# Kernel tuning notes

Hardware: AMD Instinct MI355X
Metric: run time of the kernel (lower is better)

The kernel has to match this reference:

```python
import jax, jax.numpy as jnp
import numpy as np

B, S, HID = 4, 4096, 2048
H = 16            # num_attention_heads
P = 256           # page_size
D = HID // H      # head_dim = 128
N = S // P        # num pages = 16
SCALE = D ** -0.5


def setup_inputs() -> dict:
    key = jax.random.key(0)
    ks = jax.random.split(key, 9)
    w = lambda k: (jax.random.normal(k, (HID, HID), jnp.float32) * 0.02)
    return {
        "hidden_states": jax.random.normal(ks[0], (B, S, HID), jnp.float32),
        "Wq": w(ks[1]), "bq": jnp.zeros((HID,), jnp.float32),
        "Wk": w(ks[2]), "bk": jnp.zeros((HID,), jnp.float32),
        "Wv": w(ks[3]), "bv": jnp.zeros((HID,), jnp.float32),
        "Wo": w(ks[4]), "bo": jnp.zeros((HID,), jnp.float32),
    }


def _heads(y):
    # (B,S,HID) -> (B,H,S,D)  [mirrors _reshape]
    return jnp.transpose(y.reshape(B, S, H, D), (0, 2, 1, 3))


def _paged(x):
    # torch: x.unfold(2, P, P) -> (B,H,N,D,P); then .reshape(-1,H,P,D)
    # reinterprets the row-major flat buffer. Reproduce exactly.
    u = jnp.swapaxes(x.reshape(B, H, N, P, D), -1, -2)  # (B,H,N,D,P)
    return u.reshape(B * N, H, P, D)


def reference(hidden_states, Wq, bq, Wk, bk, Wv, bv, Wo, bo):
    q = _heads(hidden_states @ Wq.T + bq)
    k = _heads(hidden_states @ Wk.T + bk)
    v = _heads(hidden_states @ Wv.T + bv)
    q, k, v = _paged(q), _paged(k), _paged(v)  # (B*N, H, P, D) each

    scores = jnp.einsum("xhqd,xhkd->xhqk", q, k) * SCALE  # (B*N,H,P,P)
    probs = jax.nn.softmax(scores, axis=-1)
    ctx = jnp.einsum("xhqk,xhkd->xhqd", probs, v)         # (B*N,H,P,D)

    # ctx.transpose(1,2).view(b, -1, hidden)
    ctx = jnp.transpose(ctx, (0, 2, 1, 3)).reshape(B, N * P, HID)
    return ctx @ Wo.T + bo
```

## Files before the change

### kernel.cpp

```cpp
#include <hip/hip_runtime.h>


typedef unsigned short u16;
typedef unsigned int u32;
typedef __attribute__((ext_vector_type(8))) __bf16 bf16x8;
typedef __attribute__((ext_vector_type(4))) float f32x4;
typedef __attribute__((ext_vector_type(8))) u16 u16x8;

struct alignas(8) U4 { u16 x, y, z, w; };

#define SCALE_ 0.08838834764831845f

__device__ __forceinline__ u16 f2bf(float f) {
  union { float f; u32 u; } v; v.f = f;
  u32 r = v.u + 0x7fffu + ((v.u >> 16) & 1u);
  return (u16)(r >> 16);
}

__device__ __forceinline__ void glds16(const void* g, void* l) {
  __builtin_amdgcn_global_load_lds(
      (const __attribute__((address_space(1))) u32*)g,
      (__attribute__((address_space(3))) u32*)l, 16, 0, 0);
}

__global__ void cvt_kernel(const float* __restrict__ src, u16* __restrict__ dst, int n4) {
  int i = blockIdx.x * 256 + threadIdx.x;
  if (i >= n4) return;
  float4 f = ((const float4*)src)[i];
  U4 o = { f2bf(f.x), f2bf(f.y), f2bf(f.z), f2bf(f.w) };
  ((U4*)dst)[i] = o;
}

__global__ void cvtw_kernel(const float* __restrict__ s0, const float* __restrict__ s1,
                            const float* __restrict__ s2, const float* __restrict__ s3,
                            u16* __restrict__ d0, int n4) {
  const int w = blockIdx.y;
  const float* src = (w == 0) ? s0 : (w == 1) ? s1 : (w == 2) ? s2 : s3;
  u16* dst = d0 + (size_t)w * 4194304;
  int i = blockIdx.x * 256 + threadIdx.x;
  if (i >= n4) return;
  float4 f = ((const float4*)src)[i];
  U4 o = { f2bf(f.x), f2bf(f.y), f2bf(f.z), f2bf(f.w) };
  ((U4*)dst)[i] = o;
}


#define MFMA_Q(AF, BF, MB, NB) do { \
  _Pragma("unroll") for (int mt_ = 0; mt_ < 4; ++mt_) \
  _Pragma("unroll") for (int nt_ = 0; nt_ < 2; ++nt_) \
  _Pragma("unroll") for (int kh_ = 0; kh_ < 2; ++kh_) \
    acc[(MB)+mt_][(NB)+nt_] = __builtin_amdgcn_mfma_f32_16x16x32_bf16( \
      AF[mt_][kh_], BF[nt_][kh_], acc[(MB)+mt_][(NB)+nt_], 0, 0, 0); \
} while (0)

#define LDA(F, MTB, BUF) do { \
  _Pragma("unroll") for (int mt_ = 0; mt_ < 4; ++mt_) { \
    F[mt_][0] = *(const bf16x8*)(aRd0 + (BUF)*65536 + ((MTB)+mt_)*2048); \
    F[mt_][1] = *(const bf16x8*)(aRd1 + (BUF)*65536 + ((MTB)+mt_)*2048); \
  } } while (0)

#define LDB(F, NTB, BUF) do { \
  _Pragma("unroll") for (int nt_ = 0; nt_ < 2; ++nt_) { \
    F[nt_][0] = *(const bf16x8*)(bRd0 + (BUF)*65536 + ((NTB)+nt_)*2048); \
    F[nt_][1] = *(const bf16x8*)(bRd1 + (BUF)*65536 + ((NTB)+nt_)*2048); \
  } } while (0)

#define STAGE_A(BUF, H, KK) do { \
  glds16(Asrc + (size_t)((H)*128) * 2048 + (KK), dstA + (BUF)*65536 + (H)*16384); \
  glds16(Asrc + (size_t)((H)*128 + 64) * 2048 + (KK), dstA + (BUF)*65536 + (H)*16384 + 8192); \
} while (0)

#define STAGE_B(BUF, H, KK) do { \
  glds16(Bsrc + (size_t)((H)*128) * 2048 + (KK), dstB + (BUF)*65536 + (H)*16384); \
  glds16(Bsrc + (size_t)((H)*128 + 64) * 2048 + (KK), dstB + (BUF)*65536 + (H)*16384 + 8192); \
} while (0)

#define PH_ENTER() do { \
  __builtin_amdgcn_s_barrier(); \
  asm volatile("s_waitcnt lgkmcnt(0)" ::: "memory"); \
  __builtin_amdgcn_sched_barrier(0); \
  __builtin_amdgcn_s_setprio(1); \
} while (0)

#define PH_EXIT() do { \
  __builtin_amdgcn_s_setprio(0); \
  __builtin_amdgcn_sched_barrier(0); \
  __builtin_amdgcn_s_barrier(); \
} while (0)

#define PH_EXIT_VM(N) do { \
  __builtin_amdgcn_s_setprio(0); \
  __builtin_amdgcn_sched_barrier(0); \
  asm volatile("s_waitcnt vmcnt(" #N ")" ::: "memory"); \
  __builtin_amdgcn_s_barrier(); \
} while (0)

#define LGKM_HINT() asm volatile("s_waitcnt lgkmcnt(8)" ::: "memory")

__global__ __launch_bounds__(512, 2) void gemm_kernel(
    const u16* __restrict__ A,
    const u16* __restrict__ W0, const u16* __restrict__ W1, const u16* __restrict__ W2,
    const float* __restrict__ b0, const float* __restrict__ b1, const float* __restrict__ b2,
    void* __restrict__ o0, void* __restrict__ o1, void* __restrict__ o2,
    int md0, int md1, int md2)
{
  extern __shared__ char Sm[];
  const int g = blockIdx.y;
  const u16* Bw     = (g == 0) ? W0 : (g == 1) ? W1 : W2;
  const float* bias = (g == 0) ? b0 : (g == 1) ? b1 : b2;
  void* outp        = (g == 0) ? o0 : (g == 1) ? o1 : o2;
  const int mode    = (g == 0) ? md0 : (g == 1) ? md1 : md2;

  const int tid  = threadIdx.x;
  const int lane = tid & 63;
  const int wid  = tid >> 6;
  const int L    = lane & 15;
  const int quad = lane >> 4;
  const int wm   = wid >> 2;
  const int wn   = wid & 3;
  const int bid = blockIdx.x;
  const int xcd = bid & 7;
  const int idx = bid >> 3;
  const int m0 = (xcd * 8 + (idx & 7)) << 8;
  const int n0 = (idx >> 3) << 8;

  const int srow = tid >> 3;
  const int scs  = (tid & 7) ^ (srow & 7);
  const u16* Asrc = A  + (size_t)(m0 + srow) * 2048 + scs * 8;
  const u16* Bsrc = Bw + (size_t)(n0 + srow) * 2048 + scs * 8;
  char* dstA = Sm + tid * 16;
  char* dstB = Sm + 32768 + tid * 16;

  const int xA = ((quad ^ (L & 7)) << 4);
  const char* aRd0 = Sm + (wm * 128 + L) * 128 + xA;
  const char* aRd1 = Sm + (wm * 128 + L) * 128 + (xA ^ 64);
  const char* bRd0 = Sm + 32768 + (wn * 64 + L) * 128 + xA;
  const char* bRd1 = Sm + 32768 + (wn * 64 + L) * 128 + (xA ^ 64);

  f32x4 acc[8][4];
#pragma unroll
  for (int i = 0; i < 8; ++i)
#pragma unroll
    for (int j = 0; j < 4; ++j)
      acc[i][j] = f32x4{0.f, 0.f, 0.f, 0.f};

  bf16x8 aLo[4][2], aHi[4][2], bLo[2][2], bHi[2][2];

  STAGE_A(0, 0, 0);
  STAGE_A(0, 1, 0);
  STAGE_B(0, 0, 0);
  STAGE_B(0, 1, 0);
  STAGE_A(1, 0, 64);
  STAGE_A(1, 1, 64);
  STAGE_B(1, 0, 64);
  STAGE_B(1, 1, 64);
  asm volatile("s_waitcnt vmcnt(8)" ::: "memory");
  __builtin_amdgcn_s_barrier();

#pragma unroll 1
  for (int it = 0; it < 16; ++it) {
    const int kb = it * 128;
    LDA(aLo, 0, 0); LDB(bLo, 0, 0);
    LGKM_HINT();
    PH_ENTER();
    MFMA_Q(aLo, bLo, 0, 0);
    PH_EXIT();
    LDA(aHi, 4, 0); LDB(bHi, 2, 0);
    LGKM_HINT();
    PH_ENTER();
    MFMA_Q(aLo, bHi, 0, 2);
    PH_EXIT();
    if (it < 15) { STAGE_A(0, 0, kb + 128); STAGE_A(0, 1, kb + 128); }
    PH_ENTER();
    MFMA_Q(aHi, bLo, 4, 0);
    PH_EXIT();
    if (it < 15) { STAGE_B(0, 0, kb + 128); STAGE_B(0, 1, kb + 128); }
    PH_ENTER();
    MFMA_Q(aHi, bHi, 4, 2);
    if (it < 15) { PH_EXIT_VM(8); } else { PH_EXIT_VM(0); }
    LDA(aLo, 0, 1); LDB(bLo, 0, 1);
    LGKM_HINT();
    PH_ENTER();
    MFMA_Q(aLo, bLo, 0, 0);
    PH_EXIT();
    LDA(aHi, 4, 1); LDB(bHi, 2, 1);
    LGKM_HINT();
    PH_ENTER();
    MFMA_Q(aLo, bHi, 0, 2);
    PH_EXIT();
    if (it < 15) { STAGE_A(1, 0, kb + 192); STAGE_A(1, 1, kb + 192); }
    PH_ENTER();
    MFMA_Q(aHi, bLo, 4, 0);
    PH_EXIT();
    if (it < 15) { STAGE_B(1, 0, kb + 192); STAGE_B(1, 1, kb + 192); }
    PH_ENTER();
    MFMA_Q(aHi, bHi, 4, 2);
    if (it < 15) { PH_EXIT_VM(8); } else { PH_EXIT(); }
  }

#pragma unroll
  for (int nt = 0; nt < 4; ++nt) {
    const int c = n0 + wn * 64 + nt * 16 + L;
    const float bv = bias[c];
    const int h = c >> 7, d = c & 127;
#pragma unroll
    for (int mt = 0; mt < 8; ++mt) {
      const int sg = m0 + wm * 128 + mt * 16 + (quad << 2);
      const int b   = sg >> 12;
      const int s   = sg & 4095;
      const int npg = (s >> 8) & 15;
      const int half = (s >> 7) & 1;
      const int plo  = s & 127;
      const f32x4 v = acc[mt][nt];
      const size_t bb = ((size_t)((b * 16 + h) * 16 + npg)) << 15;
      if (mode == 0) {
        U4 o = { f2bf(v[0] + bv), f2bf(v[1] + bv), f2bf(v[2] + bv), f2bf(v[3] + bv) };
        *(U4*)((u16*)outp + bb + (size_t)(2 * d + half) * 128 + plo) = o;
      } else if (mode == 1) {
        u16* o16 = (u16*)outp + bb + 2 * d + half;
        o16[(size_t)(plo + 0) * 256] = f2bf(v[0] + bv);
        o16[(size_t)(plo + 1) * 256] = f2bf(v[1] + bv);
        o16[(size_t)(plo + 2) * 256] = f2bf(v[2] + bv);
        o16[(size_t)(plo + 3) * 256] = f2bf(v[3] + bv);
      } else {
        float* of = (float*)outp + (size_t)sg * 2048 + c;
        of[0]    = v[0] + bv;
        of[2048] = v[1] + bv;
        of[4096] = v[2] + bv;
        of[6144] = v[3] + bv;
      }
    }
  }
}

__global__ __launch_bounds__(1024, 4) void attn_kernel(
    const u16* __restrict__ Qp, const u16* __restrict__ Kp,
    const u16* __restrict__ Vt, u16* __restrict__ ctx)
{
  __shared__ u16 Sm[32768];
  const int tid  = threadIdx.x;
  const int wid  = tid >> 6;
  const int lane = tid & 63;
  const int L    = lane & 15;
  const int quad = lane >> 4;
  const int pg   = blockIdx.x;
  const int x2 = pg >> 4, h2 = pg & 15;
  const int q0 = wid * 16;

  const char* Qb = (const char*)(Qp + (size_t)pg * 32768);
  const char* Kb = (const char*)(Kp + (size_t)pg * 32768);
  const char* Vb = (const char*)(Vt + (size_t)pg * 32768);

#pragma unroll
  for (int r = 0; r < 4; ++r) {
    const int u = tid + (r << 10);
    const int row = u >> 4, cc = u & 15;
    glds16(Kb + (size_t)(row * 16 + (cc ^ (row & 15))) * 16, (char*)Sm + u * 16);
  }

  bf16x8 qf[4];
#pragma unroll
  for (int kt = 0; kt < 4; ++kt)
    qf[kt] = *(const bf16x8*)(Qb + (q0 + L) * 256 + kt * 64 + quad * 16);

  __syncthreads();

  f32x4 st[16];
#pragma unroll
  for (int mt = 0; mt < 16; ++mt) st[mt] = f32x4{0.f, 0.f, 0.f, 0.f};
#pragma unroll
  for (int kt = 0; kt < 4; ++kt) {
    const int c = kt * 4 + quad;
#pragma unroll
    for (int mt = 0; mt < 16; ++mt) {
      bf16x8 a = *(const bf16x8*)((const char*)Sm + (mt * 16 + L) * 256 + ((c ^ L) << 4));
      st[mt] = __builtin_amdgcn_mfma_f32_16x16x32_bf16(a, qf[kt], st[mt], 0, 0, 0);
    }
  }

  float mx = -3.0e38f;
#pragma unroll
  for (int mt = 0; mt < 16; ++mt) {
    mx = fmaxf(mx, st[mt][0]); mx = fmaxf(mx, st[mt][1]);
    mx = fmaxf(mx, st[mt][2]); mx = fmaxf(mx, st[mt][3]);
  }
  mx = fmaxf(mx, __shfl_xor(mx, 16));
  mx = fmaxf(mx, __shfl_xor(mx, 32));
  float sum = 0.f;
#pragma unroll
  for (int mt = 0; mt < 16; ++mt) {
#pragma unroll
    for (int r = 0; r < 4; ++r) {
      float e = __expf((st[mt][r] - mx) * SCALE_);
      st[mt][r] = e;
      sum += e;
    }
  }
  sum += __shfl_xor(sum, 16);
  sum += __shfl_xor(sum, 32);
  const float rinv = 1.f / sum;

  __syncthreads();
#pragma unroll
  for (int r = 0; r < 4; ++r) {
    const int u = tid + (r << 10);
    const int row = u >> 5, cc = u & 31;
    glds16(Vb + (size_t)(row * 32 + (cc ^ (row & 15))) * 16, (char*)Sm + u * 16);
  }
  __syncthreads();

  f32x4 ct[8];
#pragma unroll
  for (int mt = 0; mt < 8; ++mt) ct[mt] = f32x4{0.f, 0.f, 0.f, 0.f};
#pragma unroll
  for (int kt = 0; kt < 8; ++kt) {
    u16x8 pt;
#pragma unroll
    for (int j = 0; j < 8; ++j) {
      const int src = ((quad & 1) * 2 + (j >> 2)) * 16 + L;
      float v0 = __shfl(st[2 * kt][j & 3], src);
      float v1 = __shfl(st[2 * kt + 1][j & 3], src);
      pt[j] = f2bf(quad < 2 ? v0 : v1);
    }
    bf16x8 pb = __builtin_bit_cast(bf16x8, pt);
    const int c = kt * 4 + quad;
#pragma unroll
    for (int mt = 0; mt < 8; ++mt) {
      bf16x8 a = *(const bf16x8*)((const char*)Sm + (mt * 16 + L) * 512 + ((c ^ L) << 4));
      ct[mt] = __builtin_amdgcn_mfma_f32_16x16x32_bf16(a, pb, ct[mt], 0, 0, 0);
    }
  }

  const int b = x2 >> 4, h = x2 & 15;
  const int sg = h * 256 + q0 + L;
  u16* orow = ctx + ((size_t)b * 4096 + sg) * 2048 + h2 * 128;
#pragma unroll
  for (int mt = 0; mt < 8; ++mt) {
    U4 o = { f2bf(ct[mt][0] * rinv), f2bf(ct[mt][1] * rinv),
             f2bf(ct[mt][2] * rinv), f2bf(ct[mt][3] * rinv) };
    *(U4*)(orow + mt * 16 + quad * 4) = o;
  }
}

extern "C" void kernel_launch(void* const* d_in, const int* in_sizes, int n_in,
                              void* d_out, int out_size, void* d_ws, size_t ws_size,
                              hipStream_t stream) {
  const float* X  = (const float*)d_in[0];
  const float* Wq = (const float*)d_in[1];
  const float* bq = (const float*)d_in[2];
  const float* Wk = (const float*)d_in[3];
  const float* bk = (const float*)d_in[4];
  const float* Wv = (const float*)d_in[5];
  const float* bv = (const float*)d_in[6];
  const float* Wo = (const float*)d_in[7];
  const float* bo = (const float*)d_in[8];

  static bool attr_set = false;
  if (!attr_set) {
    hipFuncSetAttribute((const void*)gemm_kernel,
                        hipFuncAttributeMaxDynamicSharedMemorySize, 131072);
    attr_set = true;
  }

  char* ws = (char*)d_ws;
  u16* Xb  = (u16*)(ws);
  u16* Wqb = (u16*)(ws + 67108864);
  u16* Qp  = (u16*)(ws + 100663296);
  u16* Kp  = (u16*)(ws + 167772160);
  u16* Vt  = (u16*)(ws + 234881024);
  u16* Cb  = (u16*)(ws + 301989888);
  u16* Wkb = Wqb + 4194304;
  u16* Wvb = Wqb + 8388608;
  u16* Wob = Wqb + 12582912;

  cvt_kernel<<<32768, 256, 0, stream>>>(X, Xb, 8388608);
  cvtw_kernel<<<dim3(4096, 4), 256, 0, stream>>>(Wq, Wk, Wv, Wo, Wqb, 1048576);

  gemm_kernel<<<dim3(512, 3), 512, 131072, stream>>>(
      Xb, Wqb, Wkb, Wvb, bq, bk, bv, (void*)Qp, (void*)Kp, (void*)Vt, 0, 0, 1);

  attn_kernel<<<1024, 1024, 0, stream>>>(Qp, Kp, Vt, Cb);

  gemm_kernel<<<dim3(512, 1), 512, 131072, stream>>>(
      Cb, Wob, Wob, Wob, bo, bo, bo, d_out, d_out, d_out, 2, 2, 2);
}
```

Baseline: 890.8 us.

## Reorder GEMM main loop MFMA quadrants to prefetch B fragments across phases

Restructures the inner K-loop of the QKV/O projection GEMM so B fragments are loaded one phase ahead and MFMA quadrants run in an order that reuses the resident A/B register fragments. The lgkmcnt hints are dropped and the global-to-LDS waits become vmcnt(0) at different points. The goal is to hide LDS read latency behind MFMA work. In exchange, the full vmcnt(0) waits may expose global load latency and serialize the staging pipeline.

```diff
diff --git a/kernel.cpp b/kernel.cpp
--- a/kernel.cpp
+++ b/kernel.cpp
@@ -94,8 +94,6 @@
   asm volatile("s_waitcnt vmcnt(" #N ")" ::: "memory"); \
   __builtin_amdgcn_s_barrier(); \
 } while (0)
-
-#define LGKM_HINT() asm volatile("s_waitcnt lgkmcnt(8)" ::: "memory")
 
 __global__ __launch_bounds__(512, 2) void gemm_kernel(
     const u16* __restrict__ A,
@@ -144,58 +142,57 @@
     for (int j = 0; j < 4; ++j)
       acc[i][j] = f32x4{0.f, 0.f, 0.f, 0.f};
 
-  bf16x8 aLo[4][2], aHi[4][2], bLo[2][2], bHi[2][2];
-
-  STAGE_A(0, 0, 0);
-  STAGE_A(0, 1, 0);
-  STAGE_B(0, 0, 0);
-  STAGE_B(0, 1, 0);
-  STAGE_A(1, 0, 64);
-  STAGE_A(1, 1, 64);
-  STAGE_B(1, 0, 64);
-  STAGE_B(1, 1, 64);
-  asm volatile("s_waitcnt vmcnt(8)" ::: "memory");
+  bf16x8 aL[4][2], aH[4][2], b0f[2][2], b1f[2][2];
+
+  STAGE_A(0, 0, 0);  STAGE_A(0, 1, 0);
+  STAGE_B(0, 0, 0);  STAGE_B(0, 1, 0);
+  STAGE_A(1, 0, 64); STAGE_A(1, 1, 64);
+  STAGE_B(1, 0, 64); STAGE_B(1, 1, 64);
+  asm volatile("s_waitcnt vmcnt(0)" ::: "memory");
   __builtin_amdgcn_s_barrier();
+  LDB(b0f, 0, 0);
 
 #pragma unroll 1
   for (int it = 0; it < 16; ++it) {
     const int kb = it * 128;
-    LDA(aLo, 0, 0); LDB(bLo, 0, 0);
-    LGKM_HINT();
-    PH_ENTER();
-    MFMA_Q(aLo, bLo, 0, 0);
-    PH_EXIT();
-    LDA(aHi, 4, 0); LDB(bHi, 2, 0);
-    LGKM_HINT();
-    PH_ENTER();
-    MFMA_Q(aLo, bHi, 0, 2);
-    PH_EXIT();
+    LDA(aL, 0, 0);
+    PH_ENTER();
+    MFMA_Q(aL, b0f, 0, 0);
+    PH_EXIT();
+    LDA(aH, 4, 0);
+    PH_ENTER();
+    MFMA_Q(aH, b0f, 4, 0);
+    PH_EXIT();
+    LDB(b1f, 2, 0);
+    PH_ENTER();
+    MFMA_Q(aH, b1f, 4, 2);
+    PH_EXIT_VM(0);
+    LDB(b0f, 0, 1);
     if (it < 15) { STAGE_A(0, 0, kb + 128); STAGE_A(0, 1, kb + 128); }
     PH_ENTER();
-    MFMA_Q(aHi, bLo, 4, 0);
-    PH_EXIT();
+    MFMA_Q(aL, b1f, 0, 2);
+    PH_EXIT();
+    LDA(aL, 0, 1);
     if (it < 15) { STAGE_B(0, 0, kb + 128); STAGE_B(0, 1, kb + 128); }
     PH_ENTER();
-    MFMA_Q(aHi, bHi, 4, 2);
-    if (it < 15) { PH_EXIT_VM(8); } else { PH_EXIT_VM(0); }
-    LDA(aLo, 0, 1); LDB(bLo, 0, 1);
-    LGKM_HINT();
-    PH_ENTER();
-    MFMA_Q(aLo, bLo, 0, 0);
-    PH_EXIT();
-    LDA(aHi, 4, 1); LDB(bHi, 2, 1);
-    LGKM_HINT();
-    PH_ENTER();
-    MFMA_Q(aLo, bHi, 0, 2);
-    PH_EXIT();
-    if (it < 15) { STAGE_A(1, 0, kb + 192); STAGE_A(1, 1, kb + 192); }
-    PH_ENTER();
-    MFMA_Q(aHi, bLo, 4, 0);
-    PH_EXIT();
-    if (it < 15) { STAGE_B(1, 0, kb + 192); STAGE_B(1, 1, kb + 192); }
-    PH_ENTER();
-    MFMA_Q(aHi, bHi, 4, 2);
-    if (it < 15) { PH_EXIT_VM(8); } else { PH_EXIT(); }
+    MFMA_Q(aL, b0f, 0, 0);
+    PH_EXIT();
+    LDA(aH, 4, 1);
+    PH_ENTER();
+    MFMA_Q(aH, b0f, 4, 0);
+    PH_EXIT();
+    LDB(b1f, 2, 1);
+    PH_ENTER();
+    MFMA_Q(aH, b1f, 4, 2);
+    PH_EXIT_VM(0);
+    if (it < 15) {
+      LDB(b0f, 0, 0);
+      STAGE_A(1, 0, kb + 192); STAGE_A(1, 1, kb + 192);
+      STAGE_B(1, 0, kb + 192); STAGE_B(1, 1, kb + 192);
+    }
+    PH_ENTER();
+    MFMA_Q(aL, b1f, 0, 2);
+    PH_EXIT();
   }
 
 #pragma unroll
```

New measurement: 874.9 us. No clear change (-1.8%).
